# Kernel tuning notes

Measured on AMD Instinct MI355X. Metric: run time of the kernel, lower is better.

## Reference

```python
import jax, jax.numpy as jnp
import numpy as np

BLOCK = 32          # Q4_0 block size
Q_ZERO = 8.0        # 4-bit zero point


def setup_inputs() -> dict:
    key = jax.random.key(0)
    k1, k2, k3, k4 = jax.random.split(key, 4)
    O, I = 8192, 8192
    nb = I // BLOCK                      # 256 blocks per row
    x = jax.random.normal(k1, (4096, I), dtype=jnp.float32)
    # packed Q4_0 payload: 16 bytes per block, each byte holds two 4-bit quants
    qweight = jax.random.randint(k2, (O, nb, BLOCK // 2), 0, 256, dtype=jnp.int32)
    scales = jax.random.uniform(k3, (O, nb), dtype=jnp.float32)
    bias = jax.random.normal(k4, (O,), dtype=jnp.float32)
    return {"x": x, "qweight": qweight, "scales": scales, "bias": bias}


def _dequantize_q4_0(qweight, scales):
    # qweight: [O, NB, 16] bytes; low nibble -> elems 0..15, high nibble -> 16..31
    O, nb, _ = qweight.shape
    low = qweight & 0xF
    high = (qweight >> 4) & 0xF
    vals = jnp.concatenate([low, high], axis=-1).astype(scales.dtype)  # [O, NB, 32]
    w = (vals - Q_ZERO) * scales[..., None]                            # [O, NB, 32]
    return w.reshape(O, nb * BLOCK)                                    # [O, I]


def reference(x, qweight, scales, bias):
    # GGUFLayer.cast_bias_weight: dequantize weight/bias to input dtype, then linear
    w = _dequantize_q4_0(qweight, scales).astype(x.dtype)  # [O, I]
    b = bias.astype(x.dtype)
    return jnp.einsum('ni,oi->no', x, w) + b               # F.linear(x, w, b)
```

## Files before the change

### kernel.cpp

```cpp
#include <hip/hip_runtime.h>
#include <stdint.h>

#define M_DIM 4096
#define N_DIM 8192
#define K_DIM 8192
#define NB    256

#define BM 256
#define BN 256
#define BK 64

typedef __attribute__((ext_vector_type(8)))  __bf16 bf16x8;
typedef __attribute__((ext_vector_type(16))) float  floatx16;
typedef __attribute__((ext_vector_type(4)))  unsigned short ushort4v;
typedef __attribute__((ext_vector_type(8)))  unsigned short ushort8;

__device__ __forceinline__ unsigned short f32_to_bf16_rne(float f) {
    union { float f; unsigned int u; } v; v.f = f;
    unsigned int u = v.u;
    u += 0x7FFFu + ((u >> 16) & 1u);
    return (unsigned short)(u >> 16);
}

__global__ __launch_bounds__(256) void dequant_w(const int* __restrict__ qw,
                                                 const float* __restrict__ sc,
                                                 unsigned short* __restrict__ w) {
    const int tid = blockIdx.x * 256 + threadIdx.x;
    const int blk = tid >> 2;
    const int q   = tid & 3;
    const int4* src = (const int4*)qw + (size_t)blk * 4 + (q & 1) * 2;
    int4 v0 = src[0];
    int4 v1 = src[1];
    const float scale = sc[blk];
    const int sh = (q >> 1) * 4;
    int by[8] = { v0.x, v0.y, v0.z, v0.w, v1.x, v1.y, v1.z, v1.w };
    ushort8 o;
#pragma unroll
    for (int j = 0; j < 8; ++j)
        o[j] = f32_to_bf16_rne((float)(((by[j] >> sh) & 0xF) - 8) * scale);
    *(ushort8*)(w + (size_t)blk * 32 + q * 8) = o;
}

__global__ __launch_bounds__(256) void convert_x(const float* __restrict__ x,
                                                 unsigned short* __restrict__ xb) {
    size_t idx = ((size_t)blockIdx.x * 256 + threadIdx.x) * 4;
    float4 f = *(const float4*)(x + idx);
    ushort4v o;
    o[0] = f32_to_bf16_rne(f.x); o[1] = f32_to_bf16_rne(f.y);
    o[2] = f32_to_bf16_rne(f.z); o[3] = f32_to_bf16_rne(f.w);
    *(ushort4v*)(xb + idx) = o;
}

__device__ __forceinline__ void load_lds16(const unsigned short* g, unsigned short* l) {
    __builtin_amdgcn_global_load_lds(
        (const __attribute__((address_space(1))) unsigned int*)(g),
        (__attribute__((address_space(3))) unsigned int*)(l),
        16, 0, 0);
}

__device__ __forceinline__ floatx16 mfma_op(bf16x8 a, bf16x8 b, floatx16 c) {
    return __builtin_amdgcn_mfma_f32_32x32x16_bf16(a, b, c, 0, 0, 0);
}

#define SL(kk, F) (((((kk) * 2) + q5) ^ (F)) * 8)

#define STAGE_A(b, h, kb) do { \
    load_lds16(gA + (size_t)((h) * 128 +  0) * K_DIM + (kb) * BK, &lsA[b][((h) * 128 +  0 + wave * 8) * BK]); \
    load_lds16(gA + (size_t)((h) * 128 + 64) * K_DIM + (kb) * BK, &lsA[b][((h) * 128 + 64 + wave * 8) * BK]); \
} while (0)
#define STAGE_B(b, h, kb) do { \
    load_lds16(gB + (size_t)((h) * 128 +  0) * K_DIM + (kb) * BK, &lsB[b][((h) * 128 +  0 + wave * 8) * BK]); \
    load_lds16(gB + (size_t)((h) * 128 + 64) * K_DIM + (kb) * BK, &lsB[b][((h) * 128 + 64 + wave * 8) * BK]); \
} while (0)

#define RD4(dst, ls, OFF, F) \
    _Pragma("unroll") for (int kk = 0; kk < 4; ++kk) \
        dst[kk] = *(const bf16x8*)(&(ls)[(OFF) + SL(kk, F)]);

#define CL(ai, av) \
    _Pragma("unroll") for (int kk = 0; kk < 4; ++kk) { \
        acc[ai][0] = mfma_op(av[kk], b0[kk], acc[ai][0]); \
        acc[ai][1] = mfma_op(av[kk], b1[kk], acc[ai][1]); \
    }

#define PH_WAIT asm volatile("s_waitcnt lgkmcnt(0)" ::: "memory"); \
                __builtin_amdgcn_sched_barrier(0)
#define SB0     __builtin_amdgcn_sched_barrier(0)
#define PRIO1   __builtin_amdgcn_s_setprio(1)
#define PRIO0   __builtin_amdgcn_s_setprio(0)
#define BAR     __builtin_amdgcn_s_barrier()

#define TILE(bb, S1, S2, S3, S4, VMW) do { \
     \
    RD4(b0, lsB[bb], aB0, F0); RD4(b1, lsB[bb], aB1, F1); RD4(a0, lsA[bb], aA0, F0); \
    S1; BAR; PH_WAIT; \
    RD4(a1, lsA[bb], aA1, F1); SB0; \
    PRIO1; CL(0, a0); PRIO0; BAR; \
     \
    S2; BAR; PH_WAIT; \
    RD4(a2, lsA[bb], aA2, F0); SB0; \
    PRIO1; CL(1, a1); PRIO0; BAR; \
     \
    S3; BAR; PH_WAIT; \
    RD4(a3, lsA[bb], aA3, F1); SB0; \
    PRIO1; CL(2, a2); PRIO0; BAR; \
     \
    S4; BAR; PH_WAIT; \
    PRIO1; CL(3, a3); PRIO0; \
    VMW; BAR; \
} while (0)

__global__ __launch_bounds__(512, 2) void gemm_bt(const unsigned short* __restrict__ A,
                                                  const unsigned short* __restrict__ B,
                                                  const float* __restrict__ bias,
                                                  float* __restrict__ C) {
    __shared__ unsigned short lsA[2][BM * BK];
    __shared__ unsigned short lsB[2][BN * BK];

    const int tid  = threadIdx.x;
    const int wave = tid >> 6;
    const int lane = tid & 63;
    const int wm = wave >> 2;
    const int wn = wave & 3;

    const int bid = blockIdx.x;
    const int x8  = bid & 7;
    const int j   = bid >> 3;
    const int m0 = (x8 * 2 + (j >> 5)) * BM;
    const int n0 = (j & 31) * BN;

    const int lrow = lane >> 3;
    const int l7s  = lane & 7;
    const int csrc = ((l7s ^ lrow ^ wave) & 7) * 8;
    const unsigned short* gA = A + (size_t)(m0 + wave * 8 + lrow) * K_DIM + csrc;
    const unsigned short* gB = B + (size_t)(n0 + wave * 8 + lrow) * K_DIM + csrc;

    const int q5  = lane >> 5;
    const int r31 = lane & 31;
    const int l7  = lane & 7;
    const int rh  = r31 >> 3;
    const int aA0 = (wm * 128 +  0 + r31) * BK;
    const int aA1 = (wm * 128 + 32 + r31) * BK;
    const int aA2 = (wm * 128 + 64 + r31) * BK;
    const int aA3 = (wm * 128 + 96 + r31) * BK;
    const int aB0 = (wn * 64  +  0 + r31) * BK;
    const int aB1 = (wn * 64  + 32 + r31) * BK;
    const int F0  = l7 ^ (rh & 7);
    const int F1  = l7 ^ ((4 + rh) & 7);

    floatx16 acc[4][2] = {};
    bf16x8 a0[4], a1[4], a2[4], a3[4], b0[4], b1[4];

    STAGE_B(0, 0, 0); STAGE_B(0, 1, 0);
    STAGE_A(0, 0, 0); STAGE_A(0, 1, 0);
    STAGE_B(1, 0, 1); STAGE_B(1, 1, 1);
    asm volatile("s_waitcnt vmcnt(4)" ::: "memory");
    BAR;

    for (int i = 0; i < 63; ++i) {
        const int t0 = 2 * i;
        TILE(0, STAGE_A(1, 0, t0 + 1), STAGE_A(1, 1, t0 + 1),
                STAGE_B(0, 0, t0 + 2), STAGE_B(0, 1, t0 + 2),
                asm volatile("s_waitcnt vmcnt(4)" ::: "memory"));
        TILE(1, STAGE_A(0, 0, t0 + 2), STAGE_A(0, 1, t0 + 2),
                STAGE_B(1, 0, t0 + 3), STAGE_B(1, 1, t0 + 3),
                asm volatile("s_waitcnt vmcnt(4)" ::: "memory"));
    }
    TILE(0, STAGE_A(1, 0, 127), STAGE_A(1, 1, 127), (void)0, (void)0,
            asm volatile("s_waitcnt vmcnt(0)" ::: "memory"));
    TILE(1, (void)0, (void)0, (void)0, (void)0, (void)0);

#pragma unroll
    for (int fj = 0; fj < 2; ++fj) {
        const int col = n0 + wn * 64 + fj * 32 + r31;
        const float bv = bias[col];
#pragma unroll
        for (int fi = 0; fi < 4; ++fi) {
            const int rowbase = m0 + wm * 128 + fi * 32 + q5 * 4;
            const floatx16 av = acc[fi][fj];
#pragma unroll
            for (int r = 0; r < 16; ++r) {
                const int row = rowbase + (r & 3) + 8 * (r >> 2);
                C[(size_t)row * N_DIM + col] = av[r] + bv;
            }
        }
    }
}

extern "C" void kernel_launch(void* const* d_in, const int* in_sizes, int n_in,
                              void* d_out, int out_size, void* d_ws, size_t ws_size,
                              hipStream_t stream) {
    (void)in_sizes; (void)n_in; (void)out_size; (void)ws_size;
    const float* x    = (const float*)d_in[0];
    const int*   qw   = (const int*)d_in[1];
    const float* sc   = (const float*)d_in[2];
    const float* bias = (const float*)d_in[3];
    float* out = (float*)d_out;

    unsigned short* Wb = (unsigned short*)d_ws;
    unsigned short* Xb = (unsigned short*)((char*)d_ws + (size_t)N_DIM * K_DIM * 2);

    dequant_w<<<dim3((N_DIM * NB * 4) / 256), dim3(256), 0, stream>>>(qw, sc, Wb);
    convert_x<<<dim3((size_t)M_DIM * K_DIM / (256 * 4)), dim3(256), 0, stream>>>(x, Xb);
    gemm_bt<<<dim3((M_DIM / BM) * (N_DIM / BN)), dim3(512), 0, stream>>>(Xb, Wb, bias, out);
}
```

Before: 859.5 us.

## Front-load LDS fragment reads in GEMM tile and regroup MFMA phases

Each tile now reads all A and B fragments from LDS in one burst near its start, with a single lgkmcnt wait, instead of interleaving one A read with each compute phase. The MFMA phases are regrouped so each phase does two A subtiles against one B fragment, which removes three per-phase LDS waits and schedule barriers. The workgroup-to-tile mapping is also changed to a different XCD-aware swizzle. This front-loading keeps more fragments live in registers at once, which raises register pressure, and the interleave between LDS reads and MFMA issue changes.

```diff
diff --git a/kernel.cpp b/kernel.cpp
--- a/kernel.cpp
+++ b/kernel.cpp
@@ -77,36 +77,33 @@
     _Pragma("unroll") for (int kk = 0; kk < 4; ++kk) \
         dst[kk] = *(const bf16x8*)(&(ls)[(OFF) + SL(kk, F)]);
 
-#define CL(ai, av) \
+#define CL2(ai0, ai1, av0, av1, bv, jj) \
     _Pragma("unroll") for (int kk = 0; kk < 4; ++kk) { \
-        acc[ai][0] = mfma_op(av[kk], b0[kk], acc[ai][0]); \
-        acc[ai][1] = mfma_op(av[kk], b1[kk], acc[ai][1]); \
+        acc[ai0][jj] = mfma_op(av0[kk], bv[kk], acc[ai0][jj]); \
+        acc[ai1][jj] = mfma_op(av1[kk], bv[kk], acc[ai1][jj]); \
     }
 
-#define PH_WAIT asm volatile("s_waitcnt lgkmcnt(0)" ::: "memory"); \
-                __builtin_amdgcn_sched_barrier(0)
-#define SB0     __builtin_amdgcn_sched_barrier(0)
 #define PRIO1   __builtin_amdgcn_s_setprio(1)
 #define PRIO0   __builtin_amdgcn_s_setprio(0)
 #define BAR     __builtin_amdgcn_s_barrier()
 
 #define TILE(bb, S1, S2, S3, S4, VMW) do { \
      \
-    RD4(b0, lsB[bb], aB0, F0); RD4(b1, lsB[bb], aB1, F1); RD4(a0, lsA[bb], aA0, F0); \
-    S1; BAR; PH_WAIT; \
-    RD4(a1, lsA[bb], aA1, F1); SB0; \
-    PRIO1; CL(0, a0); PRIO0; BAR; \
-     \
-    S2; BAR; PH_WAIT; \
-    RD4(a2, lsA[bb], aA2, F0); SB0; \
-    PRIO1; CL(1, a1); PRIO0; BAR; \
-     \
-    S3; BAR; PH_WAIT; \
-    RD4(a3, lsA[bb], aA3, F1); SB0; \
-    PRIO1; CL(2, a2); PRIO0; BAR; \
-     \
-    S4; BAR; PH_WAIT; \
-    PRIO1; CL(3, a3); PRIO0; \
+    RD4(b0, lsB[bb], aB0, F0); RD4(a0v, lsA[bb], aA0, F0); RD4(a1v, lsA[bb], aA1, F1); \
+    S1; BAR; \
+    asm volatile("s_waitcnt lgkmcnt(0)" ::: "memory"); \
+    RD4(b1, lsB[bb], aB1, F1); RD4(a2v, lsA[bb], aA2, F0); RD4(a3v, lsA[bb], aA3, F1); \
+    __builtin_amdgcn_sched_barrier(0); \
+    PRIO1; CL2(0, 1, a0v, a1v, b0, 0); PRIO0; BAR; \
+     \
+    S2; BAR; \
+    PRIO1; CL2(0, 1, a0v, a1v, b1, 1); PRIO0; BAR; \
+     \
+    S3; BAR; \
+    PRIO1; CL2(2, 3, a2v, a3v, b0, 0); PRIO0; BAR; \
+     \
+    S4; BAR; \
+    PRIO1; CL2(2, 3, a2v, a3v, b1, 1); PRIO0; \
     VMW; BAR; \
 } while (0)
 
@@ -124,10 +121,9 @@
     const int wn = wave & 3;
 
     const int bid = blockIdx.x;
-    const int x8  = bid & 7;
-    const int j   = bid >> 3;
-    const int m0 = (x8 * 2 + (j >> 5)) * BM;
-    const int n0 = (j & 31) * BN;
+    const int wg  = (bid & 7) * 64 + (bid >> 3);
+    const int m0 = (wg >> 5) * BM;
+    const int n0 = (wg & 31) * BN;
 
     const int lrow = lane >> 3;
     const int l7s  = lane & 7;
@@ -149,7 +145,7 @@
     const int F1  = l7 ^ ((4 + rh) & 7);
 
     floatx16 acc[4][2] = {};
-    bf16x8 a0[4], a1[4], a2[4], a3[4], b0[4], b1[4];
+    bf16x8 a0v[4], a1v[4], a2v[4], a3v[4], b0[4], b1[4];
 
     STAGE_B(0, 0, 0); STAGE_B(0, 1, 0);
     STAGE_A(0, 0, 0); STAGE_A(0, 1, 0);
```

Result: slower. 876.9 us (+2.0%).
